# Kernel tuning notes

Measured on AMD Instinct MI355X. Metric: run time of the kernel, lower is better.

Reference implementation:

```python
import jax, jax.numpy as jnp
import numpy as np

# static config (matches init_kwargs / input_specs)
B, S, D, H, DH = 4, 2048, 2048, 16, 128
MAX_LEN = 1024  # round_up_to_multiple_of_256(max ragged length); lengths below max at 1024
ROPE_BASE = 10000.0


def setup_inputs() -> dict:
    key = jax.random.key(0)
    ks = jax.random.split(key, 8)
    q_src = jax.random.normal(ks[0], (B, MAX_LEN, D), jnp.float32)
    k_src = jax.random.normal(ks[1], (B, S, D), jnp.float32)
    v_src = jax.random.normal(ks[2], (B, S, D), jnp.float32)
    std = 1.0 / np.sqrt(D)
    Wq = jax.random.normal(ks[3], (D, H * DH), jnp.float32) * std
    Wk = jax.random.normal(ks[4], (D, H * DH), jnp.float32) * std
    Wv = jax.random.normal(ks[5], (D, H * DH), jnp.float32) * std
    Wo = jax.random.normal(ks[6], (H * DH, D), jnp.float32) * (1.0 / np.sqrt(H * DH))
    # mask[0]: causal bool [B,S,S]; mask[1]: full position ids [B,S]
    mask0 = jnp.broadcast_to(jnp.tril(jnp.ones((S, S), bool)), (B, S, S))
    pos_full = jnp.broadcast_to(jnp.arange(S, dtype=jnp.int32), (B, S))
    # ragged skip_mask: row i keeps lengths[i] random positions (max 1024 -> MAX_LEN)
    lengths = jnp.array([1024, 896, 768, 640], jnp.int32)
    scores = jax.random.uniform(ks[7], (B, S))
    ranks = jnp.argsort(jnp.argsort(scores, axis=1), axis=1)
    skip_mask = ranks < lengths[:, None]
    return {"q_src": q_src, "k_src": k_src, "v_src": v_src,
            "Wq": Wq, "Wk": Wk, "Wv": Wv, "Wo": Wo,
            "mask0": mask0, "pos_full": pos_full, "skip_mask": skip_mask}


def _rope(x, positions):
    # x: [B,H,L,DH], positions: [B,L] int -> rotary embedding on full head dim
    dh = x.shape[-1]
    inv_freq = 1.0 / (ROPE_BASE ** (jnp.arange(0, dh, 2, dtype=jnp.float32) / dh))
    freqs = positions.astype(jnp.float32)[:, :, None] * inv_freq      # [B,L,dh/2]
    emb = jnp.concatenate([freqs, freqs], axis=-1)[:, None]           # [B,1,L,dh]
    x1, x2 = jnp.split(x, 2, axis=-1)
    rot = jnp.concatenate([-x2, x1], axis=-1)                         # rotate_half
    return x * jnp.cos(emb) + rot * jnp.sin(emb)


def reference(q_src, k_src, v_src, Wq, Wk, Wv, Wo, mask0, pos_full, skip_mask):
    def heads(x, W):
        y = x @ W
        return y.reshape(x.shape[0], x.shape[1], H, DH).transpose(0, 2, 1, 3)

    q = heads(q_src, Wq)   # [B,H,MAX_LEN,DH]
    k = heads(k_src, Wk)   # [B,H,S,DH]
    v = heads(v_src, Wv)   # [B,H,S,DH]

    # _trim_attention_mask: gather kept rows (True-first, stable order), pad to MAX_LEN
    order = jnp.argsort(jnp.where(skip_mask, 0, 1), axis=1)[:, :MAX_LEN]  # [B,MAX_LEN]
    n = skip_mask.sum(axis=1)                                             # ragged lengths
    valid = jnp.arange(MAX_LEN)[None, :] < n[:, None]                     # [B,MAX_LEN]
    amask = jnp.take_along_axis(mask0, order[:, :, None], axis=1) & valid[:, :, None]
    pos_trim = jnp.where(valid, jnp.take_along_axis(pos_full, order, axis=1), 0)

    # RoPE: trimmed positions for q, full positions for k
    q = _rope(q, pos_trim)
    k = _rope(k, pos_full)

    # masked SDPA; fully-masked (padded) query rows -> zero output
    logits = jnp.einsum('bhld,bhsd->bhls', q, k) / np.sqrt(DH).astype(np.float32)
    logits = jnp.where(amask[:, None], logits, jnp.finfo(logits.dtype).min)
    probs = jax.nn.softmax(logits, axis=-1) * valid[:, None, :, None]
    ctx = jnp.einsum('bhls,bhsd->bhld', probs, v)                         # [B,H,MAX_LEN,DH]

    out = ctx.transpose(0, 2, 1, 3).reshape(B, MAX_LEN, H * DH) @ Wo     # [B,MAX_LEN,D]
    return out
```

## Files before the change

kernel.cpp:

```cpp
#include <hip/hip_runtime.h>

#define BB 4
#define SS 2048
#define DD 2048
#define HH 16
#define DHD 128
#define MAXL 1024

typedef __bf16 bf16x8 __attribute__((ext_vector_type(8)));
typedef float f32x4 __attribute__((ext_vector_type(4)));
typedef unsigned int u32_as1 __attribute__((address_space(1)));
typedef unsigned int u32_as3 __attribute__((address_space(3)));

__device__ __forceinline__ unsigned short f2bf(float f) {
  unsigned int u = __builtin_bit_cast(unsigned int, f);
  u += 0x7fffu + ((u >> 16) & 1u);
  return (unsigned short)(u >> 16);
}
__device__ __forceinline__ float bf2f(unsigned short h) {
  unsigned int u = ((unsigned int)h) << 16;
  return __builtin_bit_cast(float, u);
}
union U4 { uint4 u; bf16x8 b; };
__device__ __forceinline__ bf16x8 ldfrag(const unsigned short* p) {
  U4 x; x.u = *(const uint4*)p; return x.b;
}
__device__ __forceinline__ void gl_lds16(const void* g, void* l) {
  __builtin_amdgcn_global_load_lds((const u32_as1*)g, (u32_as3*)l, 16, 0, 0);
}

__global__ void build_pos(const int* __restrict__ skip, int* __restrict__ posk,
                          int* __restrict__ nval) {
  int b = blockIdx.x, t = threadIdx.x;
  __shared__ int cnts[64], offs[64];
  const int* row = skip + b * SS;
  int c = 0;
  for (int i = 0; i < 32; i++) c += (row[t * 32 + i] != 0);
  cnts[t] = c;
  __syncthreads();
  if (t == 0) {
    int run = 0;
    for (int i = 0; i < 64; i++) { offs[i] = run; run += cnts[i]; }
    nval[b] = run > MAXL ? MAXL : run;
  }
  __syncthreads();
  int o = offs[t];
  for (int i = 0; i < 32; i++)
    if (row[t * 32 + i]) { if (o < MAXL) posk[b * MAXL + o] = t * 32 + i; o++; }
  int nb = nval[b];
  for (int l = nb + t; l < MAXL; l += 64) posk[b * MAXL + l] = -1;
}

__global__ __launch_bounds__(256) void cvt3(const float* __restrict__ q,
                                            const float* __restrict__ k,
                                            const float* __restrict__ v,
                                            unsigned short* __restrict__ oq,
                                            unsigned short* __restrict__ ok,
                                            unsigned short* __restrict__ ov) {
  const int nq = BB * MAXL * DD / 4, nk = BB * SS * DD / 4;
  int idx = blockIdx.x * 256 + threadIdx.x;
  const float* src; unsigned short* dst; int off;
  if (idx < nq) { src = q; dst = oq; off = idx; }
  else if (idx < nq + nk) { src = k; dst = ok; off = idx - nq; }
  else { src = v; dst = ov; off = idx - nq - nk; }
  float4 vv = ((const float4*)src)[off];
  ushort4 h;
  h.x = f2bf(vv.x); h.y = f2bf(vv.y); h.z = f2bf(vv.z); h.w = f2bf(vv.w);
  ((ushort4*)dst)[off] = h;
}

__global__ __launch_bounds__(256) void transpose_w4(const float* __restrict__ w0,
    const float* __restrict__ w1, const float* __restrict__ w2, const float* __restrict__ w3,
    unsigned short* __restrict__ o0, unsigned short* __restrict__ o1,
    unsigned short* __restrict__ o2, unsigned short* __restrict__ o3) {
  __shared__ __align__(16) unsigned short tile[64 * 76];
  const float* W; unsigned short* Wt;
  switch (blockIdx.z) {
    case 0: W = w0; Wt = o0; break;
    case 1: W = w1; Wt = o1; break;
    case 2: W = w2; Wt = o2; break;
    default: W = w3; Wt = o3; break;
  }
  int tx = threadIdx.x;
  int K0 = blockIdx.y * 64, N0 = blockIdx.x * 64;
  #pragma unroll
  for (int i = 0; i < 4; i++) {
    int r = (tx >> 4) + i * 16, c4 = (tx & 15) * 4;
    float4 v = *(const float4*)&W[(size_t)(K0 + r) * DD + N0 + c4];
    ushort4 h;
    h.x = f2bf(v.x); h.y = f2bf(v.y); h.z = f2bf(v.z); h.w = f2bf(v.w);
    *(ushort4*)&tile[r * 76 + c4] = h;
  }
  __syncthreads();
  #pragma unroll
  for (int i = 0; i < 4; i++) {
    int n = (tx >> 4) + i * 16, k4 = (tx & 15) * 4;
    ushort4 h;
    h.x = tile[(k4 + 0) * 76 + n];
    h.y = tile[(k4 + 1) * 76 + n];
    h.z = tile[(k4 + 2) * 76 + n];
    h.w = tile[(k4 + 3) * 76 + n];
    *(ushort4*)&Wt[(size_t)(N0 + n) * DD + K0 + k4] = h;
  }
}

__global__ __launch_bounds__(512, 2) void gemm256(const unsigned short* __restrict__ A,
                                                  const unsigned short* __restrict__ Bt,
                                                  void* __restrict__ Cp,
                                                  int M, int N, int K, int mode, int Lbits) {
  __shared__ __align__(16) unsigned short lds[65536];

  const int tid = threadIdx.x;
  const int lane = tid & 63, quad = lane >> 4, c = lane & 15;
  const int w = tid >> 6;
  const int wm = (w >> 2) * 128, wn = (w & 3) * 64;

  const int nwg = gridDim.x * gridDim.y;
  const int bid0 = blockIdx.y * gridDim.x + blockIdx.x;
  const int cpx = nwg >> 3;
  const int bid = (bid0 & 7) * cpx + (bid0 >> 3);
  const int bx = bid % gridDim.x;
  const int by = bid / gridDim.x;
  const size_t tm = (size_t)by * 256, tn = (size_t)bx * 256;

  f32x4 acc[8][4] = {};

  const int trow = tid >> 3;
  const int tch = ((tid & 7) ^ (trow & 7)) * 8;
  const unsigned short* gA = A + (tm + trow) * (size_t)K + tch;
  const unsigned short* gB = Bt + (tn + trow) * (size_t)K + tch;

  auto STAGE = [&](unsigned short* asd, unsigned short* bsd, int kk) {
    #pragma unroll
    for (int i = 0; i < 4; i++) {
      gl_lds16(gA + kk + (size_t)(i * 64) * K, asd + i * 4096 + tid * 8);
      gl_lds16(gB + kk + (size_t)(i * 64) * K, bsd + i * 4096 + tid * 8);
    }
  };

  const int nkt = K >> 6;
  STAGE(lds, lds + 32768, 0);

  for (int t = 0; t < nkt; ++t) {
    const int sel = t & 1;
    const unsigned short* as = lds + sel * 16384;
    const unsigned short* bs = lds + 32768 + sel * 16384;
    if (t + 1 < nkt) {
      const int s2 = sel ^ 1;
      STAGE(lds + s2 * 16384, lds + 32768 + s2 * 16384, (t + 1) << 6);
      asm volatile("s_waitcnt vmcnt(8)" ::: "memory");
    } else {
      asm volatile("s_waitcnt vmcnt(0)" ::: "memory");
    }
    __builtin_amdgcn_s_barrier();

    bf16x8 af[4][2], ag[4][2], bfr[4][2];
    #pragma unroll
    for (int i = 0; i < 4; i++)
      #pragma unroll
      for (int ks = 0; ks < 2; ks++)
        af[i][ks] = ldfrag(&as[(wm + i * 16 + c) * 64 + (((ks * 4 + quad) ^ (c & 7)) << 3)]);
    #pragma unroll
    for (int j = 0; j < 2; j++)
      #pragma unroll
      for (int ks = 0; ks < 2; ks++)
        bfr[j][ks] = ldfrag(&bs[(wn + j * 16 + c) * 64 + (((ks * 4 + quad) ^ (c & 7)) << 3)]);
    __builtin_amdgcn_s_barrier();
    asm volatile("s_waitcnt lgkmcnt(0)" ::: "memory");
    __builtin_amdgcn_s_setprio(1);
    #pragma unroll
    for (int i = 0; i < 4; i++)
      #pragma unroll
      for (int j = 0; j < 2; j++)
        #pragma unroll
        for (int ks = 0; ks < 2; ks++)
          acc[i][j] = __builtin_amdgcn_mfma_f32_16x16x32_bf16(af[i][ks], bfr[j][ks], acc[i][j], 0, 0, 0);
    __builtin_amdgcn_s_setprio(0);
    __builtin_amdgcn_s_barrier();
    #pragma unroll
    for (int j = 2; j < 4; j++)
      #pragma unroll
      for (int ks = 0; ks < 2; ks++)
        bfr[j][ks] = ldfrag(&bs[(wn + j * 16 + c) * 64 + (((ks * 4 + quad) ^ (c & 7)) << 3)]);
    __builtin_amdgcn_s_barrier();
    asm volatile("s_waitcnt lgkmcnt(0)" ::: "memory");
    __builtin_amdgcn_s_setprio(1);
    #pragma unroll
    for (int i = 0; i < 4; i++)
      #pragma unroll
      for (int j = 2; j < 4; j++)
        #pragma unroll
        for (int ks = 0; ks < 2; ks++)
          acc[i][j] = __builtin_amdgcn_mfma_f32_16x16x32_bf16(af[i][ks], bfr[j][ks], acc[i][j], 0, 0, 0);
    __builtin_amdgcn_s_setprio(0);
    __builtin_amdgcn_s_barrier();
    #pragma unroll
    for (int i = 0; i < 4; i++)
      #pragma unroll
      for (int ks = 0; ks < 2; ks++)
        ag[i][ks] = ldfrag(&as[(wm + 64 + i * 16 + c) * 64 + (((ks * 4 + quad) ^ (c & 7)) << 3)]);
    __builtin_amdgcn_s_barrier();
    asm volatile("s_waitcnt lgkmcnt(0)" ::: "memory");
    __builtin_amdgcn_s_setprio(1);
    #pragma unroll
    for (int i = 0; i < 4; i++)
      #pragma unroll
      for (int j = 0; j < 2; j++)
        #pragma unroll
        for (int ks = 0; ks < 2; ks++)
          acc[4 + i][j] = __builtin_amdgcn_mfma_f32_16x16x32_bf16(ag[i][ks], bfr[j][ks], acc[4 + i][j], 0, 0, 0);
    __builtin_amdgcn_s_setprio(0);
    __builtin_amdgcn_s_barrier();
    __builtin_amdgcn_s_setprio(1);
    #pragma unroll
    for (int i = 0; i < 4; i++)
      #pragma unroll
      for (int j = 2; j < 4; j++)
        #pragma unroll
        for (int ks = 0; ks < 2; ks++)
          acc[4 + i][j] = __builtin_amdgcn_mfma_f32_16x16x32_bf16(ag[i][ks], bfr[j][ks], acc[4 + i][j], 0, 0, 0);
    __builtin_amdgcn_s_setprio(0);
    __builtin_amdgcn_s_barrier();
  }

  if (mode == 1) {
    float* Cf = (float*)Cp;
    #pragma unroll
    for (int i = 0; i < 8; i++)
      #pragma unroll
      for (int j = 0; j < 4; j++)
        #pragma unroll
        for (int r = 0; r < 4; r++) {
          size_t m = tm + wm + i * 16 + quad * 4 + r;
          size_t n = tn + wn + j * 16 + c;
          Cf[m * N + n] = acc[i][j][r];
        }
    return;
  }
  unsigned short* Cb = (unsigned short*)Cp;
  unsigned short* ep = lds + w * 8192;
  if (mode == 0) {
    const size_t Lmask = ((size_t)1 << Lbits) - 1;
    #pragma unroll
    for (int mh = 0; mh < 2; mh++) {
      #pragma unroll
      for (int i = 0; i < 4; i++)
        #pragma unroll
        for (int j = 0; j < 4; j++)
          #pragma unroll
          for (int r = 0; r < 4; r++)
            ep[(i * 16 + quad * 4 + r) * 68 + j * 16 + c] = f2bf(acc[mh * 4 + i][j][r]);
      #pragma unroll
      for (int it = 0; it < 8; it++) {
        int chunk = it * 64 + lane;
        int ml = chunk >> 3, nc = (chunk & 7) * 8;
        uint4 val = *(const uint4*)&ep[ml * 68 + nc];
        size_t m = tm + wm + mh * 64 + ml, n = tn + wn + nc;
        size_t b = m >> Lbits, l = m & Lmask, h = n >> 7, d = n & 127;
        *(uint4*)&Cb[(((b * HH + h) << Lbits) + l) * 128 + d] = val;
      }
    }
  } else {
    #pragma unroll
    for (int mh = 0; mh < 2; mh++) {
      #pragma unroll
      for (int i = 0; i < 4; i++)
        #pragma unroll
        for (int j = 0; j < 4; j++)
          #pragma unroll
          for (int r = 0; r < 4; r++)
            ep[(j * 16 + c) * 68 + i * 16 + quad * 4 + r] = f2bf(acc[mh * 4 + i][j][r]);
      #pragma unroll
      for (int it = 0; it < 8; it++) {
        int chunk = it * 64 + lane;
        int nl = chunk >> 3, mc = (chunk & 7) * 8;
        uint4 val = *(const uint4*)&ep[nl * 68 + mc];
        size_t n = tn + wn + nl, m = tm + wm + mh * 64 + mc;
        size_t b = m >> 11, s = m & 2047, h = n >> 7, d = n & 127;
        *(uint4*)&Cb[((b * HH + h) * 128 + d) * SS + s] = val;
      }
    }
  }
}

__global__ __launch_bounds__(256) void rope2(unsigned short* __restrict__ xq,
                                             unsigned short* __restrict__ xk,
                                             const int* __restrict__ posk) {
  const int Nq = BB * HH * MAXL * 64;
  int gid = blockIdx.x * 256 + threadIdx.x;
  unsigned short* x; int Lbits, idx, use_posk;
  if (gid < Nq) { x = xq; Lbits = 10; use_posk = 1; idx = gid; }
  else { x = xk; Lbits = 11; use_posk = 0; idx = gid - Nq; }
  int d = idx & 63;
  int rest = idx >> 6;
  int l = rest & ((1 << Lbits) - 1);
  int bh = rest >> Lbits;
  int b = bh >> 4;
  int p = use_posk ? posk[(b << 10) + l] : l;
  float ang = (float)p * __expf(-(float)d * 0.14391156831212787f);
  float sn, cs;
  __sincosf(ang, &sn, &cs);
  size_t base = (size_t)rest * 128;
  float x1 = bf2f(x[base + d]), x2 = bf2f(x[base + d + 64]);
  x[base + d]      = f2bf(x1 * cs - x2 * sn);
  x[base + d + 64] = f2bf(x2 * cs + x1 * sn);
}

__global__ __launch_bounds__(256) void attn_kernel(const unsigned short* __restrict__ qp,
                                                   const unsigned short* __restrict__ kp,
                                                   const unsigned short* __restrict__ vtp,
                                                   const int* __restrict__ posk,
                                                   const int* __restrict__ nval,
                                                   unsigned short* __restrict__ ctx) {
  __shared__ __align__(16) unsigned short k_s[64 * 128];
  __shared__ __align__(16) unsigned short vt_s[128 * 64];
  __shared__ __align__(16) unsigned short p_s[4 * 16 * 72];
  __shared__ int km_s[64];

  const int tid = threadIdx.x;
  const int w = tid >> 6, lane = tid & 63, quad = lane >> 4, c = lane & 15;
  const int bh = blockIdx.x, b = bh >> 4, h = bh & 15;
  const int qbase = blockIdx.y * 64;
  const int nb = nval[b];

  if (tid < 64) {
    int l = qbase + tid;
    km_s[tid] = (l < nb) ? posk[(b << 10) + l] : -1;
  }
  __syncthreads();

  const unsigned short* qg = qp + (((size_t)bh << 10) + qbase) * 128;
  bf16x8 aq[4];
  #pragma unroll
  for (int ks = 0; ks < 4; ks++)
    aq[ks] = ldfrag(&qg[(size_t)(w * 16 + c) * 128 + ks * 32 + quad * 8]);

  int lv = nb - 1 - qbase; lv = lv > 63 ? 63 : lv;
  const int tile_kmax = (lv >= 0) ? km_s[lv] : -1;
  const int nkt = (tile_kmax >= 0) ? ((tile_kmax >> 6) + 1) : 0;

  int km[4];
  #pragma unroll
  for (int r = 0; r < 4; r++) km[r] = km_s[w * 16 + quad * 4 + r];

  const int srow = tid >> 4;
  const int kswz = (tid & 15) ^ (srow & 7);
  const unsigned short* kgp = kp + ((size_t)bh << 11) * 128 + (size_t)srow * 128 + kswz * 8;
  const int dvrow = tid >> 3;
  const int vswz = (tid & 7) ^ (dvrow & 7);
  const unsigned short* vgp = vtp + ((size_t)bh * 128 + dvrow) * SS + vswz * 8;

  float m_i[4], l_i[4];
  #pragma unroll
  for (int r = 0; r < 4; r++) { m_i[r] = -1e30f; l_i[r] = 0.f; }
  f32x4 o[8];
  #pragma unroll
  for (int dj = 0; dj < 8; dj++) o[dj] = (f32x4){0.f, 0.f, 0.f, 0.f};

  for (int kt = 0; kt < nkt; kt++) {
    const int kb = kt * 64;
    __syncthreads();
    #pragma unroll
    for (int i = 0; i < 4; i++)
      gl_lds16(kgp + ((size_t)kb + i * 16) * 128, &k_s[(i * 256 + tid) * 8]);
    #pragma unroll
    for (int i = 0; i < 4; i++)
      gl_lds16(vgp + (size_t)kb + (size_t)i * 32 * SS, &vt_s[(i * 256 + tid) * 8]);
    __syncthreads();

    f32x4 sa[4];
    #pragma unroll
    for (int j = 0; j < 4; j++) {
      sa[j] = (f32x4){0.f, 0.f, 0.f, 0.f};
      #pragma unroll
      for (int ks = 0; ks < 4; ks++) {
        bf16x8 bk = ldfrag(&k_s[((j * 16 + c) << 7) + (((ks * 4 + quad) ^ (c & 7)) << 3)]);
        sa[j] = __builtin_amdgcn_mfma_f32_16x16x32_bf16(aq[ks], bk, sa[j], 0, 0, 0);
      }
    }

    const float scale = 0.08838834764831843f;
    float mt[4] = {-1e30f, -1e30f, -1e30f, -1e30f};
    #pragma unroll
    for (int j = 0; j < 4; j++) {
      int key = kb + j * 16 + c;
      #pragma unroll
      for (int r = 0; r < 4; r++) {
        float v = (key <= km[r]) ? sa[j][r] * scale : -1e30f;
        sa[j][r] = v;
        mt[r] = fmaxf(mt[r], v);
      }
    }
    #pragma unroll
    for (int r = 0; r < 4; r++)
      for (int off = 1; off < 16; off <<= 1)
        mt[r] = fmaxf(mt[r], __shfl_xor(mt[r], off, 16));
    float al[4], rs[4];
    #pragma unroll
    for (int r = 0; r < 4; r++) {
      float mn = fmaxf(m_i[r], mt[r]);
      al[r] = __expf(m_i[r] - mn);
      m_i[r] = mn;
      rs[r] = 0.f;
    }
    #pragma unroll
    for (int j = 0; j < 4; j++)
      #pragma unroll
      for (int r = 0; r < 4; r++) {
        float pv = __expf(sa[j][r] - m_i[r]);
        sa[j][r] = pv;
        rs[r] += pv;
      }
    #pragma unroll
    for (int r = 0; r < 4; r++) {
      for (int off = 1; off < 16; off <<= 1) rs[r] += __shfl_xor(rs[r], off, 16);
      l_i[r] = l_i[r] * al[r] + rs[r];
    }
    #pragma unroll
    for (int dj = 0; dj < 8; dj++)
      #pragma unroll
      for (int r = 0; r < 4; r++) o[dj][r] *= al[r];

    #pragma unroll
    for (int j = 0; j < 4; j++)
      #pragma unroll
      for (int r = 0; r < 4; r++)
        p_s[w * 1152 + (quad * 4 + r) * 72 + j * 16 + c] = f2bf(sa[j][r]);

    #pragma unroll
    for (int ks2 = 0; ks2 < 2; ks2++) {
      bf16x8 ap = ldfrag(&p_s[w * 1152 + c * 72 + ks2 * 32 + quad * 8]);
      #pragma unroll
      for (int dj = 0; dj < 8; dj++) {
        bf16x8 bv = ldfrag(&vt_s[((dj * 16 + c) << 6) + (((ks2 * 4 + quad) ^ (c & 7)) << 3)]);
        o[dj] = __builtin_amdgcn_mfma_f32_16x16x32_bf16(ap, bv, o[dj], 0, 0, 0);
      }
    }
  }

  #pragma unroll
  for (int r = 0; r < 4; r++) {
    int l = qbase + w * 16 + quad * 4 + r;
    bool ok = (l < nb);
    float inv = ok ? (1.0f / l_i[r]) : 0.0f;
    #pragma unroll
    for (int dj = 0; dj < 8; dj++)
      ctx[(((size_t)b << 10) + l) * (size_t)DD + h * 128 + dj * 16 + c] =
          f2bf(ok ? o[dj][r] * inv : 0.0f);
  }
}

extern "C" void kernel_launch(void* const* d_in, const int* in_sizes, int n_in,
                              void* d_out, int out_size, void* d_ws, size_t ws_size,
                              hipStream_t stream) {
  const float* q_src = (const float*)d_in[0];
  const float* k_src = (const float*)d_in[1];
  const float* v_src = (const float*)d_in[2];
  const float* Wq = (const float*)d_in[3];
  const float* Wk = (const float*)d_in[4];
  const float* Wv = (const float*)d_in[5];
  const float* Wo = (const float*)d_in[6];
  const int* skip = (const int*)d_in[9];

  char* p = (char*)d_ws;
  auto alloc = [&](size_t bytes) -> char* {
    char* r = p;
    p += (bytes + 255) & ~(size_t)255;
    return r;
  };
  unsigned short* a_q  = (unsigned short*)alloc((size_t)BB * MAXL * DD * 2);
  unsigned short* a_k  = (unsigned short*)alloc((size_t)BB * SS * DD * 2);
  unsigned short* a_v  = (unsigned short*)alloc((size_t)BB * SS * DD * 2);
  unsigned short* wt_q = (unsigned short*)alloc((size_t)DD * DD * 2);
  unsigned short* wt_k = (unsigned short*)alloc((size_t)DD * DD * 2);
  unsigned short* wt_v = (unsigned short*)alloc((size_t)DD * DD * 2);
  unsigned short* wt_o = (unsigned short*)alloc((size_t)DD * DD * 2);
  unsigned short* q_pro = (unsigned short*)alloc((size_t)BB * HH * MAXL * DHD * 2);
  unsigned short* k_pro = (unsigned short*)alloc((size_t)BB * HH * SS * DHD * 2);
  unsigned short* v_t   = (unsigned short*)alloc((size_t)BB * HH * SS * DHD * 2);
  int* posk = (int*)alloc((size_t)BB * MAXL * 4);
  int* nval = (int*)alloc(64);
  unsigned short* ctx = a_q;

  build_pos<<<BB, 64, 0, stream>>>(skip, posk, nval);
  cvt3<<<(BB * MAXL * DD + 2 * BB * SS * DD) / (4 * 256), 256, 0, stream>>>(
      q_src, k_src, v_src, a_q, a_k, a_v);
  transpose_w4<<<dim3(32, 32, 4), 256, 0, stream>>>(Wq, Wk, Wv, Wo, wt_q, wt_k, wt_v, wt_o);

  gemm256<<<dim3(8, 16), 512, 0, stream>>>(a_q, wt_q, q_pro, BB * MAXL, DD, DD, 0, 10);
  gemm256<<<dim3(8, 32), 512, 0, stream>>>(a_k, wt_k, k_pro, BB * SS, DD, DD, 0, 11);
  gemm256<<<dim3(8, 32), 512, 0, stream>>>(a_v, wt_v, v_t, BB * SS, DD, DD, 2, 11);

  rope2<<<(BB * HH * (MAXL + SS) * 64) / 256, 256, 0, stream>>>(q_pro, k_pro, posk);

  attn_kernel<<<dim3(BB * HH, MAXL / 64), 256, 0, stream>>>(q_pro, k_pro, v_t, posk, nval, ctx);

  gemm256<<<dim3(8, 16), 512, 0, stream>>>(ctx, wt_o, d_out, BB * MAXL, DD, DD, 1, 0);
}
```

Before: 763.0 us.

## Templatize GEMM tile height, double-buffer attention K/V loads, add DPP reductions

The GEMM becomes a template on M-tile height. The Q and output projections now use 128-row tiles, which doubles their grid to 256 workgroups so more CUs are busy. The attention kernel double-buffers its K/V LDS tiles with async global-to-LDS loads so the next tile's fetch overlaps the current tile's compute. It also skips per-wave work beyond that wave's causal key limit and replaces the shuffle reductions with DPP. Dropping the explicit lgkmcnt waits and shrinking the epilogue LDS stride carry correctness and synchronisation risk.

Measured after the change: 692.7 us. 1.1x faster.

```diff
diff --git a/kernel.cpp b/kernel.cpp
--- a/kernel.cpp
+++ b/kernel.cpp
@@ -27,6 +27,26 @@
 }
 __device__ __forceinline__ void gl_lds16(const void* g, void* l) {
   __builtin_amdgcn_global_load_lds((const u32_as1*)g, (u32_as3*)l, 16, 0, 0);
+}
+
+template <int C>
+__device__ __forceinline__ float dppf(float x) {
+  return __builtin_bit_cast(float,
+      __builtin_amdgcn_mov_dpp(__builtin_bit_cast(int, x), C, 0xF, 0xF, true));
+}
+__device__ __forceinline__ float rmax16(float x) {
+  x = fmaxf(x, dppf<0xB1>(x));
+  x = fmaxf(x, dppf<0x4E>(x));
+  x = fmaxf(x, dppf<0x141>(x));
+  x = fmaxf(x, dppf<0x140>(x));
+  return x;
+}
+__device__ __forceinline__ float radd16(float x) {
+  x += dppf<0xB1>(x);
+  x += dppf<0x4E>(x);
+  x += dppf<0x141>(x);
+  x += dppf<0x140>(x);
+  return x;
 }
 
 __global__ void build_pos(const int* __restrict__ skip, int* __restrict__ posk,
@@ -104,16 +124,20 @@
   }
 }
 
-__global__ __launch_bounds__(512, 2) void gemm256(const unsigned short* __restrict__ A,
-                                                  const unsigned short* __restrict__ Bt,
-                                                  void* __restrict__ Cp,
-                                                  int M, int N, int K, int mode, int Lbits) {
-  __shared__ __align__(16) unsigned short lds[65536];
+template <int BM>
+__global__ __launch_bounds__(512, 2) void gemm8(const unsigned short* __restrict__ A,
+                                                const unsigned short* __restrict__ Bt,
+                                                void* __restrict__ Cp,
+                                                int M, int N, int K, int mode, int Lbits) {
+  constexpr int AW = BM * 64;
+  __shared__ __align__(16) unsigned short lds[(BM + 256) * 64 * 2];
+  unsigned short* const Abuf = lds;
+  unsigned short* const Bbuf = lds + 2 * AW;
 
   const int tid = threadIdx.x;
   const int lane = tid & 63, quad = lane >> 4, c = lane & 15;
   const int w = tid >> 6;
-  const int wm = (w >> 2) * 128, wn = (w & 3) * 64;
+  const int wm = (w >> 2) * (BM / 2), wn = (w & 3) * 64;
 
   const int nwg = gridDim.x * gridDim.y;
   const int bid0 = blockIdx.y * gridDim.x + blockIdx.x;
@@ -121,52 +145,56 @@
   const int bid = (bid0 & 7) * cpx + (bid0 >> 3);
   const int bx = bid % gridDim.x;
   const int by = bid / gridDim.x;
-  const size_t tm = (size_t)by * 256, tn = (size_t)bx * 256;
-
-  f32x4 acc[8][4] = {};
+  const size_t tm = (size_t)by * BM, tn = (size_t)bx * 256;
+
+  constexpr int MR = BM / 32;
+  f32x4 acc[MR][4] = {};
 
   const int trow = tid >> 3;
   const int tch = ((tid & 7) ^ (trow & 7)) * 8;
   const unsigned short* gA = A + (tm + trow) * (size_t)K + tch;
   const unsigned short* gB = Bt + (tn + trow) * (size_t)K + tch;
-
-  auto STAGE = [&](unsigned short* asd, unsigned short* bsd, int kk) {
-    #pragma unroll
-    for (int i = 0; i < 4; i++) {
-      gl_lds16(gA + kk + (size_t)(i * 64) * K, asd + i * 4096 + tid * 8);
-      gl_lds16(gB + kk + (size_t)(i * 64) * K, bsd + i * 4096 + tid * 8);
-    }
+  constexpr int ALD = BM / 64;
+  constexpr int NLD = ALD + 4;
+
+  auto STAGE = [&](int sel, int kk) {
+    unsigned short* ad = Abuf + sel * AW;
+    unsigned short* bd = Bbuf + sel * 16384;
+    #pragma unroll
+    for (int i = 0; i < ALD; i++)
+      gl_lds16(gA + kk + (size_t)(i * 64) * K, ad + i * 4096 + tid * 8);
+    #pragma unroll
+    for (int i = 0; i < 4; i++)
+      gl_lds16(gB + kk + (size_t)(i * 64) * K, bd + i * 4096 + tid * 8);
   };
 
   const int nkt = K >> 6;
-  STAGE(lds, lds + 32768, 0);
+  STAGE(0, 0);
 
   for (int t = 0; t < nkt; ++t) {
     const int sel = t & 1;
-    const unsigned short* as = lds + sel * 16384;
-    const unsigned short* bs = lds + 32768 + sel * 16384;
+    const unsigned short* as = Abuf + sel * AW;
+    const unsigned short* bs = Bbuf + sel * 16384;
     if (t + 1 < nkt) {
-      const int s2 = sel ^ 1;
-      STAGE(lds + s2 * 16384, lds + 32768 + s2 * 16384, (t + 1) << 6);
-      asm volatile("s_waitcnt vmcnt(8)" ::: "memory");
+      STAGE(sel ^ 1, (t + 1) << 6);
+      asm volatile("s_waitcnt vmcnt(%0)" ::"i"(NLD) : "memory");
     } else {
       asm volatile("s_waitcnt vmcnt(0)" ::: "memory");
     }
     __builtin_amdgcn_s_barrier();
 
-    bf16x8 af[4][2], ag[4][2], bfr[4][2];
+    bf16x8 a0[4][2], b01[2][2], b23[2][2];
     #pragma unroll
     for (int i = 0; i < 4; i++)
       #pragma unroll
       for (int ks = 0; ks < 2; ks++)
-        af[i][ks] = ldfrag(&as[(wm + i * 16 + c) * 64 + (((ks * 4 + quad) ^ (c & 7)) << 3)]);
+        a0[i][ks] = ldfrag(&as[(wm + i * 16 + c) * 64 + (((ks * 4 + quad) ^ (c & 7)) << 3)]);
     #pragma unroll
     for (int j = 0; j < 2; j++)
       #pragma unroll
       for (int ks = 0; ks < 2; ks++)
-        bfr[j][ks] = ldfrag(&bs[(wn + j * 16 + c) * 64 + (((ks * 4 + quad) ^ (c & 7)) << 3)]);
-    __builtin_amdgcn_s_barrier();
-    asm volatile("s_waitcnt lgkmcnt(0)" ::: "memory");
+        b01[j][ks] = ldfrag(&bs[(wn + j * 16 + c) * 64 + (((ks * 4 + quad) ^ (c & 7)) << 3)]);
+    __builtin_amdgcn_s_barrier();
     __builtin_amdgcn_s_setprio(1);
     #pragma unroll
     for (int i = 0; i < 4; i++)
@@ -174,59 +202,61 @@
       for (int j = 0; j < 2; j++)
         #pragma unroll
         for (int ks = 0; ks < 2; ks++)
-          acc[i][j] = __builtin_amdgcn_mfma_f32_16x16x32_bf16(af[i][ks], bfr[j][ks], acc[i][j], 0, 0, 0);
+          acc[i][j] = __builtin_amdgcn_mfma_f32_16x16x32_bf16(a0[i][ks], b01[j][ks], acc[i][j], 0, 0, 0);
     __builtin_amdgcn_s_setprio(0);
     __builtin_amdgcn_s_barrier();
     #pragma unroll
-    for (int j = 2; j < 4; j++)
+    for (int j = 0; j < 2; j++)
       #pragma unroll
       for (int ks = 0; ks < 2; ks++)
-        bfr[j][ks] = ldfrag(&bs[(wn + j * 16 + c) * 64 + (((ks * 4 + quad) ^ (c & 7)) << 3)]);
-    __builtin_amdgcn_s_barrier();
-    asm volatile("s_waitcnt lgkmcnt(0)" ::: "memory");
+        b23[j][ks] = ldfrag(&bs[(wn + 32 + j * 16 + c) * 64 + (((ks * 4 + quad) ^ (c & 7)) << 3)]);
+    __builtin_amdgcn_s_barrier();
     __builtin_amdgcn_s_setprio(1);
     #pragma unroll
     for (int i = 0; i < 4; i++)
       #pragma unroll
-      for (int j = 2; j < 4; j++)
+      for (int j = 0; j < 2; j++)
         #pragma unroll
         for (int ks = 0; ks < 2; ks++)
-          acc[i][j] = __builtin_amdgcn_mfma_f32_16x16x32_bf16(af[i][ks], bfr[j][ks], acc[i][j], 0, 0, 0);
+          acc[i][2 + j] = __builtin_amdgcn_mfma_f32_16x16x32_bf16(a0[i][ks], b23[j][ks], acc[i][2 + j], 0, 0, 0);
     __builtin_amdgcn_s_setprio(0);
     __builtin_amdgcn_s_barrier();
-    #pragma unroll
-    for (int i = 0; i < 4; i++)
-      #pragma unroll
-      for (int ks = 0; ks < 2; ks++)
-        ag[i][ks] = ldfrag(&as[(wm + 64 + i * 16 + c) * 64 + (((ks * 4 + quad) ^ (c & 7)) << 3)]);
-    __builtin_amdgcn_s_barrier();
-    asm volatile("s_waitcnt lgkmcnt(0)" ::: "memory");
-    __builtin_amdgcn_s_setprio(1);
-    #pragma unroll
-    for (int i = 0; i < 4; i++)
-      #pragma unroll
-      for (int j = 0; j < 2; j++)
+
+    if constexpr (BM == 256) {
+      bf16x8 a1[4][2];
+      #pragma unroll
+      for (int i = 0; i < 4; i++)
         #pragma unroll
         for (int ks = 0; ks < 2; ks++)
-          acc[4 + i][j] = __builtin_amdgcn_mfma_f32_16x16x32_bf16(ag[i][ks], bfr[j][ks], acc[4 + i][j], 0, 0, 0);
-    __builtin_amdgcn_s_setprio(0);
-    __builtin_amdgcn_s_barrier();
-    __builtin_amdgcn_s_setprio(1);
-    #pragma unroll
-    for (int i = 0; i < 4; i++)
-      #pragma unroll
-      for (int j = 2; j < 4; j++)
-        #pragma unroll
-        for (int ks = 0; ks < 2; ks++)
-          acc[4 + i][j] = __builtin_amdgcn_mfma_f32_16x16x32_bf16(ag[i][ks], bfr[j][ks], acc[4 + i][j], 0, 0, 0);
-    __builtin_amdgcn_s_setprio(0);
-    __builtin_amdgcn_s_barrier();
+          a1[i][ks] = ldfrag(&as[(wm + 64 + i * 16 + c) * 64 + (((ks * 4 + quad) ^ (c & 7)) << 3)]);
+      __builtin_amdgcn_s_barrier();
+      __builtin_amdgcn_s_setprio(1);
+      #pragma unroll
+      for (int i = 0; i < 4; i++)
+        #pragma unroll
+        for (int j = 0; j < 2; j++)
+          #pragma unroll
+          for (int ks = 0; ks < 2; ks++)
+            acc[4 + i][j] = __builtin_amdgcn_mfma_f32_16x16x32_bf16(a1[i][ks], b01[j][ks], acc[4 + i][j], 0, 0, 0);
+      __builtin_amdgcn_s_setprio(0);
+      __builtin_amdgcn_s_barrier();
+      __builtin_amdgcn_s_setprio(1);
+      #pragma unroll
+      for (int i = 0; i < 4; i++)
+        #pragma unroll
+        for (int j = 0; j < 2; j++)
+          #pragma unroll
+          for (int ks = 0; ks < 2; ks++)
+            acc[4 + i][2 + j] = __builtin_amdgcn_mfma_f32_16x16x32_bf16(a1[i][ks], b23[j][ks], acc[4 + i][2 + j], 0, 0, 0);
+      __builtin_amdgcn_s_setprio(0);
+      __builtin_amdgcn_s_barrier();
+    }
   }
 
   if (mode == 1) {
     float* Cf = (float*)Cp;
     #pragma unroll
-    for (int i = 0; i < 8; i++)
+    for (int i = 0; i < MR; i++)
       #pragma unroll
       for (int j = 0; j < 4; j++)
         #pragma unroll
@@ -238,11 +268,12 @@
     return;
   }
   unsigned short* Cb = (unsigned short*)Cp;
-  unsigned short* ep = lds + w * 8192;
+  unsigned short* ep = lds + w * 4352;
+  constexpr int MH = BM / 128;
   if (mode == 0) {
     const size_t Lmask = ((size_t)1 << Lbits) - 1;
     #pragma unroll
-    for (int mh = 0; mh < 2; mh++) {
+    for (int mh = 0; mh < MH; mh++) {
       #pragma unroll
       for (int i = 0; i < 4; i++)
         #pragma unroll
@@ -262,7 +293,7 @@
     }
   } else {
     #pragma unroll
-    for (int mh = 0; mh < 2; mh++) {
+    for (int mh = 0; mh < MH; mh++) {
       #pragma unroll
       for (int i = 0; i < 4; i++)
         #pragma unroll
@@ -312,8 +343,8 @@
                                                    const int* __restrict__ posk,
                                                    const int* __restrict__ nval,
                                                    unsigned short* __restrict__ ctx) {
-  __shared__ __align__(16) unsigned short k_s[64 * 128];
-  __shared__ __align__(16) unsigned short vt_s[128 * 64];
+  __shared__ __align__(16) unsigned short k_s[2][64 * 128];
+  __shared__ __align__(16) unsigned short vt_s[2][128 * 64];
   __shared__ __align__(16) unsigned short p_s[4 * 16 * 72];
   __shared__ int km_s[64];
 
@@ -338,6 +369,9 @@
   int lv = nb - 1 - qbase; lv = lv > 63 ? 63 : lv;
   const int tile_kmax = (lv >= 0) ? km_s[lv] : -1;
   const int nkt = (tile_kmax >= 0) ? ((tile_kmax >> 6) + 1) : 0;
+
+  int wl = w * 16 + 15; if (wl > lv) wl = lv;
+  const int wkmax = (wl >= w * 16) ? km_s[wl] : -1;
 
   int km[4];
   #pragma unroll
@@ -350,6 +384,15 @@
   const int vswz = (tid & 7) ^ (dvrow & 7);
   const unsigned short* vgp = vtp + ((size_t)bh * 128 + dvrow) * SS + vswz * 8;
 
+  auto STG = [&](int buf, int kb) {
+    #pragma unroll
+    for (int i = 0; i < 4; i++)
+      gl_lds16(kgp + ((size_t)kb + i * 16) * 128, &k_s[buf][(i * 256 + tid) * 8]);
+    #pragma unroll
+    for (int i = 0; i < 4; i++)
+      gl_lds16(vgp + (size_t)kb + (size_t)i * 32 * SS, &vt_s[buf][(i * 256 + tid) * 8]);
+  };
+
   float m_i[4], l_i[4];
   #pragma unroll
   for (int r = 0; r < 4; r++) { m_i[r] = -1e30f; l_i[r] = 0.f; }
@@ -357,85 +400,87 @@
   #pragma unroll
   for (int dj = 0; dj < 8; dj++) o[dj] = (f32x4){0.f, 0.f, 0.f, 0.f};
 
+  if (nkt > 0) STG(0, 0);
+
   for (int kt = 0; kt < nkt; kt++) {
+    const int cur = kt & 1;
     const int kb = kt * 64;
-    __syncthreads();
-    #pragma unroll
-    for (int i = 0; i < 4; i++)
-      gl_lds16(kgp + ((size_t)kb + i * 16) * 128, &k_s[(i * 256 + tid) * 8]);
-    #pragma unroll
-    for (int i = 0; i < 4; i++)
-      gl_lds16(vgp + (size_t)kb + (size_t)i * 32 * SS, &vt_s[(i * 256 + tid) * 8]);
-    __syncthreads();
-
-    f32x4 sa[4];
-    #pragma unroll
-    for (int j = 0; j < 4; j++) {
-      sa[j] = (f32x4){0.f, 0.f, 0.f, 0.f};
-      #pragma unroll
-      for (int ks = 0; ks < 4; ks++) {
-        bf16x8 bk = ldfrag(&k_s[((j * 16 + c) << 7) + (((ks * 4 + quad) ^ (c & 7)) << 3)]);
-        sa[j] = __builtin_amdgcn_mfma_f32_16x16x32_bf16(aq[ks], bk, sa[j], 0, 0, 0);
-      }
+    if (kt + 1 < nkt) {
+      STG(cur ^ 1, kb + 64);
+      asm volatile("s_waitcnt vmcnt(8)" ::: "memory");
+    } else {
+      asm volatile("s_waitcnt vmcnt(0)" ::: "memory");
     }
-
-    const float scale = 0.08838834764831843f;
-    float mt[4] = {-1e30f, -1e30f, -1e30f, -1e30f};
-    #pragma unroll
-    for (int j = 0; j < 4; j++) {
-      int key = kb + j * 16 + c;
+    __builtin_amdgcn_s_barrier();
+
+    if (kb <= wkmax) {
+      f32x4 sa[4];
+      #pragma unroll
+      for (int j = 0; j < 4; j++) {
+        sa[j] = (f32x4){0.f, 0.f, 0.f, 0.f};
+        #pragma unroll
+        for (int ks = 0; ks < 4; ks++) {
+          bf16x8 bk = ldfrag(&k_s[cur][((j * 16 + c) << 7) + (((ks * 4 + quad) ^ (c & 7)) << 3)]);
+          sa[j] = __builtin_amdgcn_mfma_f32_16x16x32_bf16(aq[ks], bk, sa[j], 0, 0, 0);
+        }
+      }
+
+      const float scale = 0.08838834764831843f;
+      float mt[4] = {-1e30f, -1e30f, -1e30f, -1e30f};
+      #pragma unroll
+      for (int j = 0; j < 4; j++) {
+        int key = kb + j * 16 + c;
+        #pragma unroll
+        for (int r = 0; r < 4; r++) {
+          float v = (key <= km[r]) ? sa[j][r] * scale : -1e30f;
+          sa[j][r] = v;
+          mt[r] = fmaxf(mt[r], v);
+        }
+      }
+      float al[4], rs[4];
       #pragma unroll
       for (int r = 0; r < 4; r++) {
-        float v = (key <= km[r]) ? sa[j][r] * scale : -1e30f;
-        sa[j][r] = v;
-        mt[r] = fmaxf(mt[r], v);
+        mt[r] = rmax16(mt[r]);
+        float mn = fmaxf(m_i[r], mt[r]);
+        al[r] = __expf(m_i[r] - mn);
+        m_i[r] = mn;
+        rs[r] = 0.f;
+      }
+      #pragma unroll
+      for (int j = 0; j < 4; j++)
+        #pragma unroll
+        for (int r = 0; r < 4; r++) {
+          float pv = __expf(sa[j][r] - m_i[r]);
+          sa[j][r] = pv;
+          rs[r] += pv;
+        }
+      #pragma unroll
+      for (int r = 0; r < 4; r++) {
+        rs[r] = radd16(rs[r]);
+        l_i[r] = l_i[r] * al[r] + rs[r];
+      }
+      #pragma unroll
+      for (int dj = 0; dj < 8; dj++)
+        #pragma unroll
+        for (int r = 0; r < 4; r++) o[dj][r] *= al[r];
+
+      #pragma unroll
+      for (int j = 0; j < 4; j++)
+        #pragma unroll
+        for (int r = 0; r < 4; r++)
+          p_s[w * 1152 + (quad * 4 + r) * 72 + j * 16 + c] = f2bf(sa[j][r]);
+
+      #pragma unroll
+      for (int ks2 = 0; ks2 < 2; ks2++) {
+        bf16x8 ap = ldfrag(&p_s[w * 1152 + c * 72 + ks2 * 32 + quad * 8]);
+        #pragma unroll
+        for (int dj = 0; dj < 8; dj++) {
+          bf16x8 bv = ldfrag(&vt_s[cur][((dj * 16 + c) << 6) + (((ks2 * 4 + quad) ^ (c & 7)) << 3)]);
+          o[dj] = __builtin_amdgcn_mfma_f32_16x16x32_bf16(ap, bv, o[dj], 0, 0, 0);
+        }
       }
     }
-    #pragma unroll
-    for (int r = 0; r < 4; r++)
-      for (int off = 1; off < 16; off <<= 1)
-        mt[r] = fmaxf(mt[r], __shfl_xor(mt[r], off, 16));
-    float al[4], rs[4];
-    #pragma unroll
-    for (int r = 0; r < 4; r++) {
-      float mn = fmaxf(m_i[r], mt[r]);
-      al[r] = __expf(m_i[r] - mn);
-      m_i[r] = mn;
-      rs[r] = 0.f;
-    }
-    #pragma unroll
-    for (int j = 0; j < 4; j++)
-      #pragma unroll
-      for (int r = 0; r < 4; r++) {
-        float pv = __expf(sa[j][r] - m_i[r]);
-        sa[j][r] = pv;
-        rs[r] += pv;
-      }
-    #pragma unroll
-    for (int r = 0; r < 4; r++) {
-      for (int off = 1; off < 16; off <<= 1) rs[r] += __shfl_xor(rs[r], off, 16);
-      l_i[r] = l_i[r] * al[r] + rs[r];
-    }
-    #pragma unroll
-    for (int dj = 0; dj < 8; dj++)
-      #pragma unroll
-      for (int r = 0; r < 4; r++) o[dj][r] *= al[r];
-
-    #pragma unroll
-    for (int j = 0; j < 4; j++)
-      #pragma unroll
-      for (int r = 0; r < 4; r++)
-        p_s[w * 1152 + (quad * 4 + r) * 72 + j * 16 + c] = f2bf(sa[j][r]);
-
-    #pragma unroll
-    for (int ks2 = 0; ks2 < 2; ks2++) {
-      bf16x8 ap = ldfrag(&p_s[w * 1152 + c * 72 + ks2 * 32 + quad * 8]);
-      #pragma unroll
-      for (int dj = 0; dj < 8; dj++) {
-        bf16x8 bv = ldfrag(&vt_s[((dj * 16 + c) << 6) + (((ks2 * 4 + quad) ^ (c & 7)) << 3)]);
-        o[dj] = __builtin_amdgcn_mfma_f32_16x16x32_bf16(ap, bv, o[dj], 0, 0, 0);
-      }
-    }
+    __builtin_amdgcn_s_barrier();
   }
 
   #pragma unroll
@@ -487,13 +532,13 @@
       q_src, k_src, v_src, a_q, a_k, a_v);
   transpose_w4<<<dim3(32, 32, 4), 256, 0, stream>>>(Wq, Wk, Wv, Wo, wt_q, wt_k, wt_v, wt_o);
 
-  gemm256<<<dim3(8, 16), 512, 0, stream>>>(a_q, wt_q, q_pro, BB * MAXL, DD, DD, 0, 10);
-  gemm256<<<dim3(8, 32), 512, 0, stream>>>(a_k, wt_k, k_pro, BB * SS, DD, DD, 0, 11);
-  gemm256<<<dim3(8, 32), 512, 0, stream>>>(a_v, wt_v, v_t, BB * SS, DD, DD, 2, 11);
+  gemm8<128><<<dim3(8, 32), 512, 0, stream>>>(a_q, wt_q, q_pro, BB * MAXL, DD, DD, 0, 10);
+  gemm8<256><<<dim3(8, 32), 512, 0, stream>>>(a_k, wt_k, k_pro, BB * SS, DD, DD, 0, 11);
+  gemm8<256><<<dim3(8, 32), 512, 0, stream>>>(a_v, wt_v, v_t, BB * SS, DD, DD, 2, 11);
 
   rope2<<<(BB * HH * (MAXL + SS) * 64) / 256, 256, 0, stream>>>(q_pro, k_pro, posk);
 
   attn_kernel<<<dim3(BB * HH, MAXL / 64), 256, 0, stream>>>(q_pro, k_pro, v_t, posk, nval, ctx);
 
-  gemm256<<<dim3(8, 16), 512, 0, stream>>>(ctx, wt_o, d_out, BB * MAXL, DD, DD, 1, 0);
-}
+  gemm8<128><<<dim3(8, 32), 512, 0, stream>>>(ctx, wt_o, d_out, BB * MAXL, DD, DD, 1, 0);
+}
```
